# Optimization experiments

Hardware: AMD Instinct MI355X
Metric: run time of the kernel (lower is better)

The kernel has to match this reference:

```python
import jax, jax.numpy as jnp
import numpy as np
import math

NUM_HEADS = 16
GRID_SIZE = 32
NUM_BUCKETS = 32
MAX_DISTANCE = 128
EMBED_DIM = 1024


def _rel_pos_bucket(rel, num_buckets, max_distance):
    # T5-style bucketing, as written in the source (int truncation of log branch)
    is_neg = (rel < 0).astype(jnp.int32)
    rel = jnp.abs(rel)
    rel = jnp.clip(rel, 0, max_distance - 1)
    max_exact = num_buckets // 2
    log_branch = max_exact + (
        jnp.log(rel.astype(jnp.float32) / max_exact)
        / math.log(max_distance / max_exact)
        * (num_buckets - max_exact)
    ).astype(jnp.int32)
    bucket = is_neg * num_buckets + jnp.where(rel < max_exact, rel.astype(jnp.int32), log_branch)
    return bucket  # in [0, 2*num_buckets)


def setup_inputs() -> dict:
    key = jax.random.key(0)
    ks = jax.random.split(key, 9)
    B, N, D = 4, GRID_SIZE * GRID_SIZE, EMBED_DIM
    s = 0.02
    return {
        "query": jax.random.normal(ks[0], (B, N, D), jnp.float32),
        "key": jax.random.normal(ks[1], (B, N, D), jnp.float32),
        "value": jax.random.normal(ks[2], (B, N, D), jnp.float32),
        "in_proj_w": jax.random.normal(ks[3], (3 * D, D), jnp.float32) * s,
        "in_proj_b": jnp.zeros((3 * D,), jnp.float32),
        "out_proj_w": jax.random.normal(ks[4], (D, D), jnp.float32) * s,
        "out_proj_b": jnp.zeros((D,), jnp.float32),
        "rel_bias_table": jax.random.normal(ks[5], (2 * NUM_BUCKETS, NUM_HEADS), jnp.float32) * s,
    }


def reference(query, key, value, in_proj_w, in_proj_b, out_proj_w, out_proj_b, rel_bias_table):
    B, N, D = query.shape
    H = NUM_HEADS
    hd = D // H
    scaling = hd ** -0.5

    # in_proj applied to `query` only (source ignores key/value args)
    qkv = query @ in_proj_w.T + in_proj_b          # [B, N, 3D]
    q, k, v = jnp.split(qkv, 3, axis=-1)
    q = q.reshape(B, N, H, hd).transpose(0, 2, 1, 3)  # [B, H, N, hd]
    k = k.reshape(B, N, H, hd).transpose(0, 2, 1, 3)
    v = v.reshape(B, N, H, hd).transpose(0, 2, 1, 3)

    attn = jnp.einsum("bhnd,bhmd->bhnm", q, k) * scaling  # [B, H, N, N]

    # 2D relative-position bucket bias
    idx = jnp.arange(N)
    row = idx // GRID_SIZE
    col = idx % GRID_SIZE
    row_bucket = _rel_pos_bucket(row[:, None] - row[None, :], NUM_BUCKETS, MAX_DISTANCE)
    col_bucket = _rel_pos_bucket(col[:, None] - col[None, :], NUM_BUCKETS, MAX_DISTANCE)
    bias = rel_bias_table[row_bucket] + rel_bias_table[col_bucket]  # [N, N, H]
    attn = attn + bias.transpose(2, 0, 1)[None]  # [B, H, N, N]

    attn_weights = jax.nn.softmax(attn, axis=-1)
    out = jnp.einsum("bhnm,bhmd->bhnd", attn_weights, v)  # [B, H, N, hd]
    out = out.transpose(0, 2, 1, 3).reshape(B, N, D)
    out = out @ out_proj_w.T + out_proj_b
    return out, attn_weights
```

## Files before the change

kernel.cpp:

```cpp
#include <hip/hip_runtime.h>
#include <hip/hip_bf16.h>

typedef __attribute__((ext_vector_type(8))) short bf16x8;
typedef __attribute__((ext_vector_type(4))) float f32x4;
typedef __attribute__((ext_vector_type(4))) unsigned short us4;

#define MFMA16(a,b,c) __builtin_amdgcn_mfma_f32_16x16x32_bf16((a),(b),(c),0,0,0)

__device__ __forceinline__ unsigned short f2bf(float f){
  unsigned u = __builtin_bit_cast(unsigned, f);
  u += 0x7fffu + ((u>>16)&1u);
  return (unsigned short)(u>>16);
}
__device__ __forceinline__ float bf2f(unsigned short h){
  unsigned u = ((unsigned)h)<<16;
  return __builtin_bit_cast(float, u);
}
__device__ __forceinline__ void gload_lds16(const unsigned short* g, unsigned short* l){
  __builtin_amdgcn_global_load_lds((const __attribute__((address_space(1))) void*)g,
                                   (__attribute__((address_space(3))) void*)l,
                                   16, 0, 0);
}

__global__ __launch_bounds__(256) void cast_all(
    const float* __restrict__ q, const float* __restrict__ wi, const float* __restrict__ wo,
    unsigned short* __restrict__ qq, unsigned short* __restrict__ wib, unsigned short* __restrict__ wob)
{
  int i4 = (blockIdx.x*256 + threadIdx.x)*4;
  const float* src; unsigned short* dst; int off;
  if (i4 < 4194304)       { src=q;  dst=qq;  off=i4; }
  else if (i4 < 7340032)  { src=wi; dst=wib; off=i4-4194304; }
  else                    { src=wo; dst=wob; off=i4-7340032; }
  float4 v = *(const float4*)(src+off);
  us4 o; o.x=f2bf(v.x); o.y=f2bf(v.y); o.z=f2bf(v.z); o.w=f2bf(v.w);
  *(us4*)(dst+off) = o;
}

__global__ __launch_bounds__(256) void gemm_qkv(
    const unsigned short* __restrict__ A, const unsigned short* __restrict__ Bw,
    const float* __restrict__ bias,
    unsigned short* __restrict__ qo, unsigned short* __restrict__ ko, unsigned short* __restrict__ vTo)
{
  __shared__ unsigned short lA[128*64];
  __shared__ unsigned short lB[128*64];
  int tid = threadIdx.x, lane = tid&63, w = tid>>6;
  int wr = (w>>1)<<6, wc = (w&1)<<6;
  int rowT = blockIdx.y<<7, colT = blockIdx.x<<7;
  f32x4 acc[4][4] = {};
  for (int k0=0; k0<1024; k0+=64){
    #pragma unroll
    for (int it=0; it<4; ++it){
      int ci = it*256+tid; int r=ci>>3, cs=ci&7;
      int c = (cs ^ (r&7))<<3;
      gload_lds16(A + (size_t)(rowT+r)*1024 + k0 + c, &lA[ci<<3]);
    }
    #pragma unroll
    for (int it=0; it<4; ++it){
      int ci = it*256+tid; int r=ci>>3, cs=ci&7;
      int c = (cs ^ (r&7))<<3;
      gload_lds16(Bw + (size_t)(colT+r)*1024 + k0 + c, &lB[ci<<3]);
    }
    asm volatile("s_waitcnt vmcnt(0)" ::: "memory");
    __syncthreads();
    #pragma unroll
    for (int kk=0; kk<2; ++kk){
      int kc = (kk<<2) + (lane>>4);
      bf16x8 a[4], b[4];
      #pragma unroll
      for (int i=0;i<4;++i){
        int r = wr + (i<<4) + (lane&15);
        a[i] = *(const bf16x8*)&lA[(r<<6) + ((kc ^ (r&7))<<3)];
      }
      #pragma unroll
      for (int j=0;j<4;++j){
        int r = wc + (j<<4) + (lane&15);
        b[j] = *(const bf16x8*)&lB[(r<<6) + ((kc ^ (r&7))<<3)];
      }
      #pragma unroll
      for (int i=0;i<4;++i)
        #pragma unroll
        for (int j=0;j<4;++j)
          acc[i][j] = MFMA16(a[i], b[j], acc[i][j]);
    }
    __syncthreads();
  }
  int sec = colT >> 10;
  #pragma unroll
  for (int i=0;i<4;++i){
    #pragma unroll
    for (int j=0;j<4;++j){
      int cg = colT + wc + (j<<4) + (lane&15);
      int d = cg & 1023, hh = d>>6, di = d&63;
      float bsv = bias[cg];
      #pragma unroll
      for (int q=0;q<4;++q){
        int m = rowT + wr + (i<<4) + ((lane>>4)<<2) + q;
        int b = m>>10, n = m&1023;
        unsigned short bv = f2bf(acc[i][j][q] + bsv);
        size_t bh = (size_t)((b<<4) + hh);
        if (sec==0)      qo[(bh<<16) + ((size_t)n<<6) + di] = bv;
        else if (sec==1) ko[(bh<<16) + ((size_t)n<<6) + di] = bv;
        else             vTo[(bh<<16) + ((size_t)di<<10) + n] = bv;
      }
    }
  }
}

__global__ __launch_bounds__(256) void gemm_out(
    const unsigned short* __restrict__ A, const unsigned short* __restrict__ Bw,
    const float* __restrict__ bias, float* __restrict__ out)
{
  __shared__ unsigned short lA[128*64];
  __shared__ unsigned short lB[128*64];
  int tid = threadIdx.x, lane = tid&63, w = tid>>6;
  int wr = (w>>1)<<6, wc = (w&1)<<6;
  int rowT = blockIdx.y<<7, colT = blockIdx.x<<7;
  f32x4 acc[4][4] = {};
  for (int k0=0; k0<1024; k0+=64){
    #pragma unroll
    for (int it=0; it<4; ++it){
      int ci = it*256+tid; int r=ci>>3, cs=ci&7;
      int c = (cs ^ (r&7))<<3;
      gload_lds16(A + (size_t)(rowT+r)*1024 + k0 + c, &lA[ci<<3]);
    }
    #pragma unroll
    for (int it=0; it<4; ++it){
      int ci = it*256+tid; int r=ci>>3, cs=ci&7;
      int c = (cs ^ (r&7))<<3;
      gload_lds16(Bw + (size_t)(colT+r)*1024 + k0 + c, &lB[ci<<3]);
    }
    asm volatile("s_waitcnt vmcnt(0)" ::: "memory");
    __syncthreads();
    #pragma unroll
    for (int kk=0; kk<2; ++kk){
      int kc = (kk<<2) + (lane>>4);
      bf16x8 a[4], b[4];
      #pragma unroll
      for (int i=0;i<4;++i){
        int r = wr + (i<<4) + (lane&15);
        a[i] = *(const bf16x8*)&lA[(r<<6) + ((kc ^ (r&7))<<3)];
      }
      #pragma unroll
      for (int j=0;j<4;++j){
        int r = wc + (j<<4) + (lane&15);
        b[j] = *(const bf16x8*)&lB[(r<<6) + ((kc ^ (r&7))<<3)];
      }
      #pragma unroll
      for (int i=0;i<4;++i)
        #pragma unroll
        for (int j=0;j<4;++j)
          acc[i][j] = MFMA16(a[i], b[j], acc[i][j]);
    }
    __syncthreads();
  }
  #pragma unroll
  for (int i=0;i<4;++i){
    #pragma unroll
    for (int j=0;j<4;++j){
      int cg = colT + wc + (j<<4) + (lane&15);
      float bsv = bias[cg];
      #pragma unroll
      for (int q=0;q<4;++q){
        int m = rowT + wr + (i<<4) + ((lane>>4)<<2) + q;
        out[(size_t)m*1024 + cg] = acc[i][j][q] + bsv;
      }
    }
  }
}

__global__ __launch_bounds__(256) void attn_fused(
    const unsigned short* __restrict__ qbf, const unsigned short* __restrict__ kbf,
    const unsigned short* __restrict__ vT, const float* __restrict__ tbl,
    float* __restrict__ attn_out, unsigned short* __restrict__ oa)
{
  __shared__ unsigned short P[32*1024];
  __shared__ unsigned short qs[32*64];
  __shared__ float biasv[64];
  __shared__ float rsum[4][32];
  __shared__ float rinv_s[32];

  int tid=threadIdx.x, lane=tid&63, w=tid>>6;
  int bid = blockIdx.x;
  int wgid = ((bid&7)<<8) + (bid>>3);
  int pair = wgid >> 5;
  int stripe = wgid & 31;
  int h = pair & 15;
  int bg = pair >> 4;
  int nbase = stripe<<5;
  const unsigned short* qg = qbf + ((size_t)pair<<16) + ((size_t)nbase<<6);
  const unsigned short* kg = kbf + ((size_t)pair<<16);
  const unsigned short* vg = vT  + ((size_t)pair<<16);

  if (tid < 63){
    int dd = tid - 31;
    int neg = dd<0 ? 1:0;
    int a = dd<0 ? -dd : dd;
    int bkt;
    if (a<16) bkt = a;
    else bkt = 16 + (int)(__logf((float)a*(1.f/16.f)) * (16.f/__logf(8.f)));
    bkt += neg*32;
    biasv[tid] = tbl[(bkt<<4) + h];
  }
  { int r=tid>>3, cs=tid&7;
    int c = (cs ^ (r&7))<<3;
    gload_lds16(qg + (r<<6) + c, &qs[tid<<3]); }
  asm volatile("s_waitcnt vmcnt(0)" ::: "memory");
  __syncthreads();

  int x = lane&15, g = lane>>4;
  float cterm[3][4];
  #pragma unroll
  for (int s=0;s<3;++s)
    #pragma unroll
    for (int q=0;q<4;++q)
      cterm[s][q] = biasv[(g<<2) + q - x + 31 + ((s-1)<<4)];

  bf16x8 qa[2][2];
  #pragma unroll
  for (int rt=0;rt<2;++rt){
    int r = (rt<<4) + x;
    #pragma unroll
    for (int hh=0;hh<2;++hh)
      qa[rt][hh] = *(const bf16x8*)&qs[(r<<6) + ((((hh<<2)+g) ^ (r&7))<<3)];
  }

  float rs[2][4] = {};
  int colW = w<<8;
  for (int ct2=0; ct2<8; ++ct2){
    int cbb = colW + (ct2<<5);
    float rterm = biasv[stripe - (cbb>>5) + 31];
    #pragma unroll
    for (int par=0; par<2; ++par){
      int cb = cbb + (par<<4);
      int j = cb + x;
      const unsigned short* kp = kg + ((size_t)j<<6) + (g<<3);
      bf16x8 bk0 = *(const bf16x8*)kp;
      bf16x8 bk1 = *(const bf16x8*)(kp+32);
      #pragma unroll
      for (int rt=0; rt<2; ++rt){
        f32x4 acc = {};
        acc = MFMA16(qa[rt][0], bk0, acc);
        acc = MFMA16(qa[rt][1], bk1, acc);
        #pragma unroll
        for (int q=0;q<4;++q){
          int r = (rt<<4) + (g<<2) + q;
          float lg = acc[q]*0.125f + rterm + cterm[rt+1-par][q];
          float e = __expf(lg);
          rs[rt][q] += e;
          int byteoff = (r<<11) + ((((j>>3) ^ (r&7)))<<4) + ((j&7)<<1);
          *(unsigned short*)((char*)P + byteoff) = f2bf(e);
        }
      }
    }
  }
  #pragma unroll
  for (int rt=0;rt<2;++rt){
    #pragma unroll
    for (int q=0;q<4;++q){
      float v = rs[rt][q];
      v += __shfl_xor(v,1); v += __shfl_xor(v,2); v += __shfl_xor(v,4); v += __shfl_xor(v,8);
      if (x==0) rsum[w][(rt<<4)+(g<<2)+q] = v;
    }
  }
  __syncthreads();
  if (tid<32) rinv_s[tid] = 1.f/(rsum[0][tid]+rsum[1][tid]+rsum[2][tid]+rsum[3][tid]);
  __syncthreads();

  float* ao = attn_out + ((size_t)pair<<20) + ((size_t)nbase<<10);
  for (int it=0; it<16; ++it){
    int r = (it<<1) + (tid>>7);
    int c8 = (tid&127)<<3;
    int byteoff = (r<<11) + ((((c8>>3) ^ (r&7)))<<4);
    bf16x8 pv8 = *(const bf16x8*)((char*)P + byteoff);
    float ri = rinv_s[r];
    float4 o0, o1;
    o0.x = bf2f((unsigned short)pv8[0])*ri;
    o0.y = bf2f((unsigned short)pv8[1])*ri;
    o0.z = bf2f((unsigned short)pv8[2])*ri;
    o0.w = bf2f((unsigned short)pv8[3])*ri;
    o1.x = bf2f((unsigned short)pv8[4])*ri;
    o1.y = bf2f((unsigned short)pv8[5])*ri;
    o1.z = bf2f((unsigned short)pv8[6])*ri;
    o1.w = bf2f((unsigned short)pv8[7])*ri;
    *(float4*)(ao + ((size_t)r<<10) + c8)     = o0;
    *(float4*)(ao + ((size_t)r<<10) + c8 + 4) = o1;
  }

  f32x4 oacc[2] = {};
  int dbase = w<<4;
  const unsigned short* vp = vg + ((size_t)(dbase + x)<<10) + (g<<3);
  #pragma unroll 4
  for (int kc=0; kc<1024; kc+=32){
    bf16x8 bv = *(const bf16x8*)(vp + kc);
    int ck = (kc>>3) + g;
    #pragma unroll
    for (int rt=0;rt<2;++rt){
      int r = (rt<<4) + x;
      bf16x8 a = *(const bf16x8*)((char*)P + (r<<11) + ((ck ^ (r&7))<<4));
      oacc[rt] = MFMA16(a, bv, oacc[rt]);
    }
  }
  #pragma unroll
  for (int rt=0;rt<2;++rt){
    #pragma unroll
    for (int q=0;q<4;++q){
      int r = (rt<<4) + (g<<2) + q;
      float val = oacc[rt][q]*rinv_s[r];
      oa[((size_t)((bg<<10) + nbase + r)<<10) + (h<<6) + dbase + x] = f2bf(val);
    }
  }
}

extern "C" void kernel_launch(void* const* d_in, const int* in_sizes, int n_in,
                              void* d_out, int out_size, void* d_ws, size_t ws_size,
                              hipStream_t stream)
{
  const float* query = (const float*)d_in[0];
  const float* wi  = (const float*)d_in[3];
  const float* bi  = (const float*)d_in[4];
  const float* wo  = (const float*)d_in[5];
  const float* bo  = (const float*)d_in[6];
  const float* tbl = (const float*)d_in[7];

  char* ws = (char*)d_ws;
  unsigned short* qq  = (unsigned short*)(ws);
  unsigned short* wib = (unsigned short*)(ws + 8388608);
  unsigned short* wob = (unsigned short*)(ws + 14680064);
  unsigned short* qbf = (unsigned short*)(ws + 16777216);
  unsigned short* kbf = (unsigned short*)(ws + 25165824);
  unsigned short* vTb = (unsigned short*)(ws + 33554432);
  unsigned short* oa  = (unsigned short*)(ws + 41943040);

  float* out  = (float*)d_out;
  float* attn = out + 4194304;

  cast_all<<<dim3(8192), dim3(256), 0, stream>>>(query, wi, wo, qq, wib, wob);
  gemm_qkv<<<dim3(24,32), dim3(256), 0, stream>>>(qq, wib, bi, qbf, kbf, vTb);
  attn_fused<<<dim3(2048), dim3(256), 0, stream>>>(qbf, kbf, vTb, tbl, attn, oa);
  gemm_out<<<dim3(8,32), dim3(256), 0, stream>>>(oa, wob, bo, out);
}
```

Baseline: 193.0 us.

## Fuse query fp32-to-bf16 cast into QKV GEMM and double-buffer GEMM LDS tiles

The separate cast of the query activations is removed. gemm_qkv now loads fp32 query tiles into registers, converts them to bf16 and writes them into LDS itself. Both GEMMs switch to double-buffered LDS, so the next K tile is prefetched while MFMAs run on the current one. This removes a full pass writing and reading an 8MB bf16 copy and hides global load latency, at the cost of double the LDS use, which can lower occupancy. The QKV GEMM also reads the query in fp32, which is twice the bytes of A traffic per block, and that traffic is repeated across the 24 column blocks.

```diff
diff --git a/kernel.cpp b/kernel.cpp
--- a/kernel.cpp
+++ b/kernel.cpp
@@ -23,45 +23,67 @@
 }
 
 __global__ __launch_bounds__(256) void cast_all(
-    const float* __restrict__ q, const float* __restrict__ wi, const float* __restrict__ wo,
-    unsigned short* __restrict__ qq, unsigned short* __restrict__ wib, unsigned short* __restrict__ wob)
+    const float* __restrict__ wi, const float* __restrict__ wo,
+    unsigned short* __restrict__ wib, unsigned short* __restrict__ wob)
 {
   int i4 = (blockIdx.x*256 + threadIdx.x)*4;
   const float* src; unsigned short* dst; int off;
-  if (i4 < 4194304)       { src=q;  dst=qq;  off=i4; }
-  else if (i4 < 7340032)  { src=wi; dst=wib; off=i4-4194304; }
-  else                    { src=wo; dst=wob; off=i4-7340032; }
+  if (i4 < 3145728) { src=wi; dst=wib; off=i4; }
+  else              { src=wo; dst=wob; off=i4-3145728; }
   float4 v = *(const float4*)(src+off);
   us4 o; o.x=f2bf(v.x); o.y=f2bf(v.y); o.z=f2bf(v.z); o.w=f2bf(v.w);
   *(us4*)(dst+off) = o;
 }
 
 __global__ __launch_bounds__(256) void gemm_qkv(
-    const unsigned short* __restrict__ A, const unsigned short* __restrict__ Bw,
+    const float* __restrict__ Af, const unsigned short* __restrict__ Bw,
     const float* __restrict__ bias,
     unsigned short* __restrict__ qo, unsigned short* __restrict__ ko, unsigned short* __restrict__ vTo)
 {
-  __shared__ unsigned short lA[128*64];
-  __shared__ unsigned short lB[128*64];
+  __shared__ unsigned short lA[2][128*64];
+  __shared__ unsigned short lB[2][128*64];
   int tid = threadIdx.x, lane = tid&63, w = tid>>6;
   int wr = (w>>1)<<6, wc = (w&1)<<6;
   int rowT = blockIdx.y<<7, colT = blockIdx.x<<7;
   f32x4 acc[4][4] = {};
-  for (int k0=0; k0<1024; k0+=64){
-    #pragma unroll
-    for (int it=0; it<4; ++it){
-      int ci = it*256+tid; int r=ci>>3, cs=ci&7;
-      int c = (cs ^ (r&7))<<3;
-      gload_lds16(A + (size_t)(rowT+r)*1024 + k0 + c, &lA[ci<<3]);
-    }
-    #pragma unroll
-    for (int it=0; it<4; ++it){
-      int ci = it*256+tid; int r=ci>>3, cs=ci&7;
-      int c = (cs ^ (r&7))<<3;
-      gload_lds16(Bw + (size_t)(colT+r)*1024 + k0 + c, &lB[ci<<3]);
-    }
-    asm volatile("s_waitcnt vmcnt(0)" ::: "memory");
-    __syncthreads();
+  f32x4 areg[8];
+
+  #pragma unroll
+  for (int it=0; it<4; ++it){
+    int ci = it*256+tid; int r=ci>>3, cs=ci&7;
+    int c = (cs ^ (r&7))<<3;
+    const float* ap = Af + (size_t)(rowT+r)*1024 + c;
+    areg[2*it]   = *(const f32x4*)ap;
+    areg[2*it+1] = *(const f32x4*)(ap+4);
+    gload_lds16(Bw + (size_t)(colT+r)*1024 + c, &lB[0][ci<<3]);
+  }
+  asm volatile("s_waitcnt vmcnt(0)" ::: "memory");
+  #pragma unroll
+  for (int it=0; it<4; ++it){
+    int ci = it*256+tid;
+    f32x4 v0=areg[2*it], v1=areg[2*it+1];
+    us4 o0, o1;
+    o0.x=f2bf(v0.x); o0.y=f2bf(v0.y); o0.z=f2bf(v0.z); o0.w=f2bf(v0.w);
+    o1.x=f2bf(v1.x); o1.y=f2bf(v1.y); o1.z=f2bf(v1.z); o1.w=f2bf(v1.w);
+    *(us4*)&lA[0][ci<<3]     = o0;
+    *(us4*)&lA[0][(ci<<3)+4] = o1;
+  }
+  __syncthreads();
+
+  for (int t=0; t<16; ++t){
+    int buf = t&1, nb = buf^1;
+    if (t < 15){
+      int k1 = (t+1)<<6;
+      #pragma unroll
+      for (int it=0; it<4; ++it){
+        int ci = it*256+tid; int r=ci>>3, cs=ci&7;
+        int c = (cs ^ (r&7))<<3;
+        const float* ap = Af + (size_t)(rowT+r)*1024 + k1 + c;
+        areg[2*it]   = *(const f32x4*)ap;
+        areg[2*it+1] = *(const f32x4*)(ap+4);
+        gload_lds16(Bw + (size_t)(colT+r)*1024 + k1 + c, &lB[nb][ci<<3]);
+      }
+    }
     #pragma unroll
     for (int kk=0; kk<2; ++kk){
       int kc = (kk<<2) + (lane>>4);
@@ -69,12 +91,12 @@
       #pragma unroll
       for (int i=0;i<4;++i){
         int r = wr + (i<<4) + (lane&15);
-        a[i] = *(const bf16x8*)&lA[(r<<6) + ((kc ^ (r&7))<<3)];
+        a[i] = *(const bf16x8*)&lA[buf][(r<<6) + ((kc ^ (r&7))<<3)];
       }
       #pragma unroll
       for (int j=0;j<4;++j){
         int r = wc + (j<<4) + (lane&15);
-        b[j] = *(const bf16x8*)&lB[(r<<6) + ((kc ^ (r&7))<<3)];
+        b[j] = *(const bf16x8*)&lB[buf][(r<<6) + ((kc ^ (r&7))<<3)];
       }
       #pragma unroll
       for (int i=0;i<4;++i)
@@ -82,8 +104,22 @@
         for (int j=0;j<4;++j)
           acc[i][j] = MFMA16(a[i], b[j], acc[i][j]);
     }
+    if (t < 15){
+      asm volatile("s_waitcnt vmcnt(0)" ::: "memory");
+      #pragma unroll
+      for (int it=0; it<4; ++it){
+        int ci = it*256+tid;
+        f32x4 v0=areg[2*it], v1=areg[2*it+1];
+        us4 o0, o1;
+        o0.x=f2bf(v0.x); o0.y=f2bf(v0.y); o0.z=f2bf(v0.z); o0.w=f2bf(v0.w);
+        o1.x=f2bf(v1.x); o1.y=f2bf(v1.y); o1.z=f2bf(v1.z); o1.w=f2bf(v1.w);
+        *(us4*)&lA[nb][ci<<3]     = o0;
+        *(us4*)&lA[nb][(ci<<3)+4] = o1;
+      }
+    }
     __syncthreads();
   }
+
   int sec = colT >> 10;
   #pragma unroll
   for (int i=0;i<4;++i){
@@ -110,27 +146,35 @@
     const unsigned short* __restrict__ A, const unsigned short* __restrict__ Bw,
     const float* __restrict__ bias, float* __restrict__ out)
 {
-  __shared__ unsigned short lA[128*64];
-  __shared__ unsigned short lB[128*64];
+  __shared__ unsigned short lA[2][128*64];
+  __shared__ unsigned short lB[2][128*64];
   int tid = threadIdx.x, lane = tid&63, w = tid>>6;
   int wr = (w>>1)<<6, wc = (w&1)<<6;
   int rowT = blockIdx.y<<7, colT = blockIdx.x<<7;
   f32x4 acc[4][4] = {};
-  for (int k0=0; k0<1024; k0+=64){
-    #pragma unroll
-    for (int it=0; it<4; ++it){
-      int ci = it*256+tid; int r=ci>>3, cs=ci&7;
-      int c = (cs ^ (r&7))<<3;
-      gload_lds16(A + (size_t)(rowT+r)*1024 + k0 + c, &lA[ci<<3]);
-    }
-    #pragma unroll
-    for (int it=0; it<4; ++it){
-      int ci = it*256+tid; int r=ci>>3, cs=ci&7;
-      int c = (cs ^ (r&7))<<3;
-      gload_lds16(Bw + (size_t)(colT+r)*1024 + k0 + c, &lB[ci<<3]);
-    }
-    asm volatile("s_waitcnt vmcnt(0)" ::: "memory");
-    __syncthreads();
+
+  #pragma unroll
+  for (int it=0; it<4; ++it){
+    int ci = it*256+tid; int r=ci>>3, cs=ci&7;
+    int c = (cs ^ (r&7))<<3;
+    gload_lds16(A  + (size_t)(rowT+r)*1024 + c, &lA[0][ci<<3]);
+    gload_lds16(Bw + (size_t)(colT+r)*1024 + c, &lB[0][ci<<3]);
+  }
+  asm volatile("s_waitcnt vmcnt(0)" ::: "memory");
+  __syncthreads();
+
+  for (int t=0; t<16; ++t){
+    int buf = t&1, nb = buf^1;
+    if (t < 15){
+      int k1 = (t+1)<<6;
+      #pragma unroll
+      for (int it=0; it<4; ++it){
+        int ci = it*256+tid; int r=ci>>3, cs=ci&7;
+        int c = (cs ^ (r&7))<<3;
+        gload_lds16(A  + (size_t)(rowT+r)*1024 + k1 + c, &lA[nb][ci<<3]);
+        gload_lds16(Bw + (size_t)(colT+r)*1024 + k1 + c, &lB[nb][ci<<3]);
+      }
+    }
     #pragma unroll
     for (int kk=0; kk<2; ++kk){
       int kc = (kk<<2) + (lane>>4);
@@ -138,12 +182,12 @@
       #pragma unroll
       for (int i=0;i<4;++i){
         int r = wr + (i<<4) + (lane&15);
-        a[i] = *(const bf16x8*)&lA[(r<<6) + ((kc ^ (r&7))<<3)];
+        a[i] = *(const bf16x8*)&lA[buf][(r<<6) + ((kc ^ (r&7))<<3)];
       }
       #pragma unroll
       for (int j=0;j<4;++j){
         int r = wc + (j<<4) + (lane&15);
-        b[j] = *(const bf16x8*)&lB[(r<<6) + ((kc ^ (r&7))<<3)];
+        b[j] = *(const bf16x8*)&lB[buf][(r<<6) + ((kc ^ (r&7))<<3)];
       }
       #pragma unroll
       for (int i=0;i<4;++i)
@@ -151,8 +195,10 @@
         for (int j=0;j<4;++j)
           acc[i][j] = MFMA16(a[i], b[j], acc[i][j]);
     }
+    if (t < 15) asm volatile("s_waitcnt vmcnt(0)" ::: "memory");
     __syncthreads();
   }
+
   #pragma unroll
   for (int i=0;i<4;++i){
     #pragma unroll
@@ -323,7 +369,6 @@
   const float* tbl = (const float*)d_in[7];
 
   char* ws = (char*)d_ws;
-  unsigned short* qq  = (unsigned short*)(ws);
   unsigned short* wib = (unsigned short*)(ws + 8388608);
   unsigned short* wob = (unsigned short*)(ws + 14680064);
   unsigned short* qbf = (unsigned short*)(ws + 16777216);
@@ -334,8 +379,8 @@
   float* out  = (float*)d_out;
   float* attn = out + 4194304;
 
-  cast_all<<<dim3(8192), dim3(256), 0, stream>>>(query, wi, wo, qq, wib, wob);
-  gemm_qkv<<<dim3(24,32), dim3(256), 0, stream>>>(qq, wib, bi, qbf, kbf, vTb);
+  cast_all<<<dim3(4096), dim3(256), 0, stream>>>(wi, wo, wib, wob);
+  gemm_qkv<<<dim3(24,32), dim3(256), 0, stream>>>(query, wib, bi, qbf, kbf, vTb);
   attn_fused<<<dim3(2048), dim3(256), 0, stream>>>(qbf, kbf, vTb, tbl, attn, oa);
   gemm_out<<<dim3(8,32), dim3(256), 0, stream>>>(oa, wob, bo, out);
 }
```

New measurement: 211.8 us. 1.1x slower.
